# Kernel tuning notes

Hardware: AMD Instinct MI355X
Metric: run time of the kernel (lower is better)

The kernel has to match this reference:

```python
import jax, jax.numpy as jnp
import numpy as np


def _gcn_norm(edge_index, num_nodes, dtype):
    # PyG GCNConv.norm: add self-loops (weight 1), symmetric deg^{-1/2} normalization
    row, col = edge_index[0], edge_index[1]
    loop = jnp.arange(num_nodes, dtype=row.dtype)
    row = jnp.concatenate([row, loop])
    col = jnp.concatenate([col, loop])
    ew = jnp.ones(row.shape[0], dtype=dtype)
    deg = jax.ops.segment_sum(ew, row, num_segments=num_nodes)
    dis = jnp.where(deg > 0, jax.lax.rsqrt(deg), 0.0)
    norm = dis[row] * ew * dis[col]
    return row, col, norm


def _masked_gcn_conv(x, row, col, norm, sigma, W, b, num_nodes):
    # mask_features: edge gather -> diff/sigma -> square -> scatter-add -> exp mask
    h = (x[col] - x[row]) / sigma            # [E, F]
    h = norm[:, None] * h * h                # [E, F]
    mask = jax.ops.segment_sum(h, row, num_segments=num_nodes)        # [N, F]
    deg = jax.ops.segment_sum(jnp.ones_like(norm), row, num_segments=num_nodes)  # degree(source), >=1 due to self-loops
    x = x * jnp.exp(-mask / deg[:, None])
    # GCNConv: linear transform then normalized aggregation source->target
    xw = x @ W                               # [N, O]
    out = jax.ops.segment_sum(norm[:, None] * xw[row], col, num_segments=num_nodes)
    return out + b


def setup_inputs() -> dict:
    key = jax.random.key(0)
    ks = jax.random.split(key, 8)
    N, E, F, H, C = 100000, 1600000, 128, 64, 40
    g = 1.414  # xavier gain used for sigma
    return {
        "x": jax.random.normal(ks[0], (N, F), jnp.float32),
        "edge_index": jax.random.randint(ks[1], (2, E), 0, N, jnp.int64),
        "sigma1": jax.random.uniform(ks[2], (1, F), jnp.float32, -1.0, 1.0) * (g * np.sqrt(6.0 / (1 + F))),
        "W1": jax.random.normal(ks[3], (F, H), jnp.float32) * (1.0 / np.sqrt(F)),
        "b1": jnp.zeros((H,), jnp.float32),
        "sigma2": jax.random.uniform(ks[4], (1, H), jnp.float32, -1.0, 1.0) * (g * np.sqrt(6.0 / (1 + H))),
        "W2": jax.random.normal(ks[5], (H, C), jnp.float32) * (1.0 / np.sqrt(H)),
        "b2": jnp.zeros((C,), jnp.float32),
    }


def reference(x, edge_index, sigma1, W1, b1, sigma2, W2, b2):
    N = x.shape[0]
    row, col, norm = _gcn_norm(edge_index, N, x.dtype)
    x = _masked_gcn_conv(x, row, col, norm, sigma1, W1, b1, N)
    x = jax.nn.relu(x)
    # dropout is identity in eval mode
    x = _masked_gcn_conv(x, row, col, norm, sigma2, W2, b2, N)
    return jax.nn.log_softmax(x, axis=1)
```

## Files before the change

### kernel.cpp

```cpp
#include <hip/hip_runtime.h>
#include <cmath>

constexpr int F1 = 128;
constexpr int H  = 64;
constexpr int NC = 40;
constexpr int NPART = 8;

constexpr int SCAN_TPB = 256;
constexpr int SCAN_IPT = 8;
constexpr int SCAN_EPB = SCAN_TPB * SCAN_IPT;

__device__ inline unsigned short f2bf(float f) {
    union { float f; unsigned u; } v; v.f = f;
    return (unsigned short)((v.u + 0x7FFFu + ((v.u >> 16) & 1u)) >> 16);
}
__device__ inline float bflo(unsigned p) { union { float f; unsigned u; } v; v.u = p << 16; return v.f; }
__device__ inline float bfhi(unsigned p) { union { float f; unsigned u; } v; v.u = p & 0xFFFF0000u; return v.f; }
__device__ inline void unpack8(uint4 raw, float* d) {
    d[0] = bflo(raw.x); d[1] = bfhi(raw.x); d[2] = bflo(raw.y); d[3] = bfhi(raw.y);
    d[4] = bflo(raw.z); d[5] = bfhi(raw.z); d[6] = bflo(raw.w); d[7] = bfhi(raw.w);
}

__device__ inline unsigned f2q(float f) {
    union { float f; unsigned u; } v; v.f = f;
    unsigned s = (v.u >> 24) & 0x80u;
    float a = fabsf(f);
    if (a > 448.0f) return s | 0x7Eu;
    if (a < 0.0009765625f) return s;
    if (a >= 0.015625f) {
        unsigned b = v.u & 0x7fffffffu;
        unsigned r = b + 0x0007FFFFu + ((b >> 20) & 1u);
        unsigned e8 = (r >> 23) - 120u;
        unsigned m8 = (r >> 20) & 7u;
        unsigned q = (e8 << 3) | m8;
        if (q > 0x7Eu) q = 0x7Eu;
        return s | q;
    }
    unsigned m = (unsigned)rintf(a * 512.0f);
    if (m > 7u) m = 8u;
    return s | m;
}
#if defined(__has_builtin) && __has_builtin(__builtin_amdgcn_cvt_pk_f32_fp8)
typedef float __attribute__((ext_vector_type(2))) f32x2_t;
__device__ inline void q2f4(unsigned w, float* d) {
    f32x2_t lo = __builtin_amdgcn_cvt_pk_f32_fp8((int)w, false);
    f32x2_t hi = __builtin_amdgcn_cvt_pk_f32_fp8((int)w, true);
    d[0] = lo[0]; d[1] = lo[1]; d[2] = hi[0]; d[3] = hi[1];
}
#else
__device__ inline float q2f1(unsigned b) {
    unsigned em = b & 0x7fu;
    union { float f; unsigned u; } r;
    r.u = (em << 20) + (120u << 23);
    float mag = em ? r.f : 0.0f;
    union { float f; unsigned u; } o; o.f = mag;
    o.u |= (b & 0x80u) << 24;
    return o.f;
}
__device__ inline void q2f4(unsigned w, float* d) {
    d[0] = q2f1(w & 0xffu); d[1] = q2f1((w >> 8) & 0xffu);
    d[2] = q2f1((w >> 16) & 0xffu); d[3] = q2f1((w >> 24) & 0xffu);
}
#endif
__device__ inline void unpackq8(uint2 raw, float* d) {
    q2f4(raw.x, d); q2f4(raw.y, d + 4);
}

__global__ void isg_kernel(const float* __restrict__ s1, float* __restrict__ i1,
                           const float* __restrict__ s2, float* __restrict__ i2) {
    int i = threadIdx.x;
    if (i < F1) i1[i] = 1.0f / s1[i];
    if (i < H)  i2[i] = 1.0f / s2[i];
}

__global__ void count8_prep_kernel(const int* __restrict__ row, const int* __restrict__ col,
                                   int* __restrict__ cntO, int* __restrict__ cntI,
                                   int E, int chunk, int stride, int cntBlocks,
                                   const float* __restrict__ x, const float* __restrict__ isg,
                                   unsigned short* __restrict__ u, unsigned char* __restrict__ uq,
                                   size_t n8) {
    int bid = blockIdx.x;
    if (bid < cntBlocks) {
        int p = bid & (NPART - 1);
        int gid = bid / NPART;
        unsigned lo = (unsigned)(p * chunk);
        for (int e = gid * blockDim.x + threadIdx.x; e < E; e += stride) {
            int r = row[e], c = col[e];
            if ((unsigned)r - lo < (unsigned)chunk) atomicAdd(&cntO[r], 1);
            if ((unsigned)c - lo < (unsigned)chunk) atomicAdd(&cntI[c], 1);
        }
    } else {
        size_t idx = (size_t)(bid - cntBlocks) * blockDim.x + threadIdx.x;
        if (idx >= n8) return;
        size_t base = idx * 8;
        int fk = (int)(base % (size_t)F1);
        float4 a0 = *(const float4*)&x[base];
        float4 a1 = *(const float4*)&x[base + 4];
        float4 s0 = *(const float4*)&isg[fk];
        float4 s1 = *(const float4*)&isg[fk + 4];
        float uv[8] = {a0.x * s0.x, a0.y * s0.y, a0.z * s0.z, a0.w * s0.w,
                       a1.x * s1.x, a1.y * s1.y, a1.z * s1.z, a1.w * s1.w};
        uint4 p4;
        p4.x = (unsigned)f2bf(uv[0]) | ((unsigned)f2bf(uv[1]) << 16);
        p4.y = (unsigned)f2bf(uv[2]) | ((unsigned)f2bf(uv[3]) << 16);
        p4.z = (unsigned)f2bf(uv[4]) | ((unsigned)f2bf(uv[5]) << 16);
        p4.w = (unsigned)f2bf(uv[6]) | ((unsigned)f2bf(uv[7]) << 16);
        *(uint4*)&u[base] = p4;
        uint2 q2;
        q2.x = f2q(uv[0]) | (f2q(uv[1]) << 8) | (f2q(uv[2]) << 16) | (f2q(uv[3]) << 24);
        q2.y = f2q(uv[4]) | (f2q(uv[5]) << 8) | (f2q(uv[6]) << 16) | (f2q(uv[7]) << 24);
        *(uint2*)&uq[base] = q2;
    }
}

__global__ void scan_partial_kernel(const int* __restrict__ cnt, int* __restrict__ bsum, int M) {
    __shared__ int red[SCAN_TPB];
    int t = threadIdx.x;
    int i0 = blockIdx.x * SCAN_EPB + t * SCAN_IPT;
    int s = 0;
#pragma unroll
    for (int k = 0; k < SCAN_IPT; ++k) {
        int i = i0 + k;
        if (i < M) s += cnt[i];
    }
    red[t] = s;
    __syncthreads();
    for (int off = SCAN_TPB / 2; off > 0; off >>= 1) {
        if (t < off) red[t] += red[t + off];
        __syncthreads();
    }
    if (t == 0) bsum[blockIdx.x] = red[0];
}

__global__ void scan_offsets_kernel(int* __restrict__ bsum, int nb,
                                    int* __restrict__ rowptrO, int* __restrict__ rowptrI,
                                    int N, int E) {
    __shared__ int sh[1024];
    int t = threadIdx.x;
    sh[t] = (t < nb) ? bsum[t] : 0;
    __syncthreads();
    for (int off = 1; off < 1024; off <<= 1) {
        int v = (t >= off) ? sh[t - off] : 0;
        __syncthreads();
        sh[t] += v;
        __syncthreads();
    }
    if (t < nb) bsum[t] = (t > 0) ? sh[t - 1] : 0;
    if (t == 0) { rowptrO[N] = E; rowptrI[N] = E; }
}

__global__ void scan_final_kernel(int* __restrict__ cntO, int* __restrict__ cntI,
                                  const int* __restrict__ bsum,
                                  int* __restrict__ rowptrO, int* __restrict__ rowptrI,
                                  float* __restrict__ dis, int N, int E) {
    __shared__ int sh[SCAN_TPB];
    int t = threadIdx.x;
    int M = 2 * N;
    const int* cnt = cntO;
    int i0 = blockIdx.x * SCAN_EPB + t * SCAN_IPT;
    int cv[SCAN_IPT], pre[SCAN_IPT];
    int run = 0;
#pragma unroll
    for (int k = 0; k < SCAN_IPT; ++k) {
        int i = i0 + k;
        cv[k] = (i < M) ? cnt[i] : 0;
        pre[k] = run;
        run += cv[k];
    }
    sh[t] = run;
    __syncthreads();
    for (int off = 1; off < SCAN_TPB; off <<= 1) {
        int v = (t >= off) ? sh[t - off] : 0;
        __syncthreads();
        sh[t] += v;
        __syncthreads();
    }
    int toff = ((t > 0) ? sh[t - 1] : 0) + bsum[blockIdx.x];
#pragma unroll
    for (int k = 0; k < SCAN_IPT; ++k) {
        int i = i0 + k;
        if (i < M) {
            int val = toff + pre[k];
            if (i < N) {
                rowptrO[i] = val;
                cntO[i] = val;
                dis[i] = rsqrtf((float)(cv[k] + 1));
            } else {
                rowptrI[i - N] = val - E;
                cntI[i - N] = val - E;
            }
        }
    }
}

__global__ void build8_kernel(const int* __restrict__ row, const int* __restrict__ col,
                              int* __restrict__ curO, int* __restrict__ curI,
                              int2* __restrict__ adjO2, int2* __restrict__ adjI2,
                              const float* __restrict__ dis,
                              int E, int chunk, int stride) {
    int p = blockIdx.x & (NPART - 1);
    int gid = blockIdx.x / NPART;
    unsigned lo = (unsigned)(p * chunk);
    for (int e = gid * blockDim.x + threadIdx.x; e < E; e += stride) {
        int r = row[e], c = col[e];
        bool inR = (unsigned)r - lo < (unsigned)chunk;
        bool inC = (unsigned)c - lo < (unsigned)chunk;
        if (inR | inC) {
            float nrm = dis[r] * dis[c];
            int nb = __float_as_int(nrm);
            if (inR) adjO2[atomicAdd(&curO[r], 1)] = make_int2(c, nb);
            if (inC) adjI2[atomicAdd(&curI[c], 1)] = make_int2(r, nb);
        }
    }
}

template<int F, int O, int R>
__global__ void fused_mask_gemm_kernel(const int* __restrict__ rowptr, const int2* __restrict__ adj2,
                                       const float* __restrict__ sig,
                                       const unsigned short* __restrict__ u,
                                       const unsigned char* __restrict__ uq,
                                       const float* __restrict__ W,
                                       unsigned short* __restrict__ Ybf, int N) {
    constexpr int NT = R * 64;
    constexpr int G = F / 8;
    constexpr int NPI = 64 / G;
    __shared__ __align__(16) float Ws[F * O];
    __shared__ __align__(16) float Xs[R][F];
    int tid = threadIdx.x;
    for (int i = tid; i < F * O; i += NT) Ws[i] = W[i];
    int w = tid >> 6, lane = tid & 63;
    int h = lane / G, j = lane % G;
    int base = blockIdx.x * R;
    int r = base + w;
    if (r < N) {
        int beg = rowptr[r], end = rowptr[r + 1];
        float inv_deg = 1.0f / (float)(end - beg + 1);
        float ur[8], acc[8];
        unpack8(*(const uint4*)&u[(size_t)r * F + 8 * j], ur);
#pragma unroll
        for (int k = 0; k < 8; ++k) acc[k] = 0.0f;
        for (int t = beg; t < end; t += 2 * NPI) {
            int e0 = t + h, e1 = t + NPI + h;
            int2 a0 = adj2[min(e0, end - 1)];
            int2 a1 = adj2[min(e1, end - 1)];
            float n0 = (e0 < end) ? __int_as_float(a0.y) : 0.0f;
            float n1 = (e1 < end) ? __int_as_float(a1.y) : 0.0f;
            uint2 rw0 = *(const uint2*)&uq[(size_t)a0.x * F + 8 * j];
            uint2 rw1 = *(const uint2*)&uq[(size_t)a1.x * F + 8 * j];
            float uc[8];
            unpackq8(rw0, uc);
#pragma unroll
            for (int q = 0; q < 8; ++q) {
                float d = uc[q] - ur[q];
                acc[q] = fmaf(n0 * d, d, acc[q]);
            }
            unpackq8(rw1, uc);
#pragma unroll
            for (int q = 0; q < 8; ++q) {
                float d = uc[q] - ur[q];
                acc[q] = fmaf(n1 * d, d, acc[q]);
            }
        }
#pragma unroll
        for (int off = G; off < 64; off <<= 1) {
#pragma unroll
            for (int k = 0; k < 8; ++k) acc[k] += __shfl_xor(acc[k], off);
        }
        if (h == 0) {
            float4 s0 = *(const float4*)&sig[8 * j];
            float4 s1 = *(const float4*)&sig[8 * j + 4];
            float sg[8] = {s0.x, s0.y, s0.z, s0.w, s1.x, s1.y, s1.z, s1.w};
            float xm[8];
#pragma unroll
            for (int k = 0; k < 8; ++k) xm[k] = ur[k] * sg[k] * expf(-acc[k] * inv_deg);
            *(float4*)&Xs[w][8 * j]     = make_float4(xm[0], xm[1], xm[2], xm[3]);
            *(float4*)&Xs[w][8 * j + 4] = make_float4(xm[4], xm[5], xm[6], xm[7]);
        }
    } else if (h == 0) {
        *(float4*)&Xs[w][8 * j]     = make_float4(0.f, 0.f, 0.f, 0.f);
        *(float4*)&Xs[w][8 * j + 4] = make_float4(0.f, 0.f, 0.f, 0.f);
    }
    __syncthreads();
    if (w < 2) {
        int r0 = base + 4 * w;
        if (r0 < N && lane < O) {
            float a0 = 0.f, a1 = 0.f, a2 = 0.f, a3 = 0.f;
#pragma unroll
            for (int fq = 0; fq < F / 4; ++fq) {
                float4 x0 = *(const float4*)&Xs[4 * w + 0][4 * fq];
                float4 x1 = *(const float4*)&Xs[4 * w + 1][4 * fq];
                float4 x2 = *(const float4*)&Xs[4 * w + 2][4 * fq];
                float4 x3 = *(const float4*)&Xs[4 * w + 3][4 * fq];
                float w0 = Ws[(4 * fq + 0) * O + lane];
                float w1 = Ws[(4 * fq + 1) * O + lane];
                float w2 = Ws[(4 * fq + 2) * O + lane];
                float w3 = Ws[(4 * fq + 3) * O + lane];
                a0 = fmaf(x0.x, w0, a0); a0 = fmaf(x0.y, w1, a0); a0 = fmaf(x0.z, w2, a0); a0 = fmaf(x0.w, w3, a0);
                a1 = fmaf(x1.x, w0, a1); a1 = fmaf(x1.y, w1, a1); a1 = fmaf(x1.z, w2, a1); a1 = fmaf(x1.w, w3, a1);
                a2 = fmaf(x2.x, w0, a2); a2 = fmaf(x2.y, w1, a2); a2 = fmaf(x2.z, w2, a2); a2 = fmaf(x2.w, w3, a2);
                a3 = fmaf(x3.x, w0, a3); a3 = fmaf(x3.y, w1, a3); a3 = fmaf(x3.z, w2, a3); a3 = fmaf(x3.w, w3, a3);
            }
            float o0 = __shfl_xor(a0, 1);
            float o1 = __shfl_xor(a1, 1);
            float o2 = __shfl_xor(a2, 1);
            float o3 = __shfl_xor(a3, 1);
            if (!(lane & 1)) {
                *(unsigned*)&Ybf[(size_t)r0 * O + lane] = (unsigned)f2bf(a0) | ((unsigned)f2bf(o0) << 16);
                if (r0 + 1 < N) *(unsigned*)&Ybf[(size_t)(r0 + 1) * O + lane] = (unsigned)f2bf(a1) | ((unsigned)f2bf(o1) << 16);
                if (r0 + 2 < N) *(unsigned*)&Ybf[(size_t)(r0 + 2) * O + lane] = (unsigned)f2bf(a2) | ((unsigned)f2bf(o2) << 16);
                if (r0 + 3 < N) *(unsigned*)&Ybf[(size_t)(r0 + 3) * O + lane] = (unsigned)f2bf(a3) | ((unsigned)f2bf(o3) << 16);
            }
        }
    }
}

__global__ void agg_relu_kernel(const int* __restrict__ rowptr, const int2* __restrict__ adj2,
                                const float* __restrict__ dis, const unsigned short* __restrict__ ybf,
                                const float* __restrict__ bias,
                                unsigned short* __restrict__ u2, unsigned char* __restrict__ u2q,
                                const float* __restrict__ isg2, int N) {
    int c = blockIdx.x * (blockDim.x >> 6) + (threadIdx.x >> 6);
    if (c >= N) return;
    int lane = threadIdx.x & 63;
    int h = lane >> 3, j = lane & 7;
    int beg = rowptr[c], end = rowptr[c + 1];
    float acc[8];
#pragma unroll
    for (int k = 0; k < 8; ++k) acc[k] = 0.0f;
    for (int t = beg; t < end; t += 16) {
        int e0 = t + h, e1 = t + 8 + h;
        int2 a0 = adj2[min(e0, end - 1)];
        int2 a1 = adj2[min(e1, end - 1)];
        float n0 = (e0 < end) ? __int_as_float(a0.y) : 0.0f;
        float n1 = (e1 < end) ? __int_as_float(a1.y) : 0.0f;
        uint4 rw0 = *(const uint4*)&ybf[(size_t)a0.x * H + 8 * j];
        uint4 rw1 = *(const uint4*)&ybf[(size_t)a1.x * H + 8 * j];
        float v[8];
        unpack8(rw0, v);
#pragma unroll
        for (int q = 0; q < 8; ++q) acc[q] = fmaf(n0, v[q], acc[q]);
        unpack8(rw1, v);
#pragma unroll
        for (int q = 0; q < 8; ++q) acc[q] = fmaf(n1, v[q], acc[q]);
    }
#pragma unroll
    for (int off = 8; off < 64; off <<= 1) {
#pragma unroll
        for (int k = 0; k < 8; ++k) acc[k] += __shfl_xor(acc[k], off);
    }
    if (h == 0) {
        float dc = dis[c];
        float sv[8];
        unpack8(*(const uint4*)&ybf[(size_t)c * H + 8 * j], sv);
        float4 b0 = *(const float4*)&bias[8 * j];
        float4 b1v = *(const float4*)&bias[8 * j + 4];
        float bb[8] = {b0.x, b0.y, b0.z, b0.w, b1v.x, b1v.y, b1v.z, b1v.w};
        float4 s0 = *(const float4*)&isg2[8 * j];
        float4 s1 = *(const float4*)&isg2[8 * j + 4];
        float sg[8] = {s0.x, s0.y, s0.z, s0.w, s1.x, s1.y, s1.z, s1.w};
        float uv[8];
        float d2 = dc * dc;
#pragma unroll
        for (int k = 0; k < 8; ++k) {
            float hv = fmaxf(fmaf(d2, sv[k], acc[k]) + bb[k], 0.0f);
            uv[k] = hv * sg[k];
        }
        uint4 p;
        p.x = (unsigned)f2bf(uv[0]) | ((unsigned)f2bf(uv[1]) << 16);
        p.y = (unsigned)f2bf(uv[2]) | ((unsigned)f2bf(uv[3]) << 16);
        p.z = (unsigned)f2bf(uv[4]) | ((unsigned)f2bf(uv[5]) << 16);
        p.w = (unsigned)f2bf(uv[6]) | ((unsigned)f2bf(uv[7]) << 16);
        *(uint4*)&u2[(size_t)c * H + 8 * j] = p;
        uint2 q2;
        q2.x = f2q(uv[0]) | (f2q(uv[1]) << 8) | (f2q(uv[2]) << 16) | (f2q(uv[3]) << 24);
        q2.y = f2q(uv[4]) | (f2q(uv[5]) << 8) | (f2q(uv[6]) << 16) | (f2q(uv[7]) << 24);
        *(uint2*)&u2q[(size_t)c * H + 8 * j] = q2;
    }
}

__global__ void agg_lsm_kernel(const int* __restrict__ rowptr, const int2* __restrict__ adj2,
                               const float* __restrict__ dis, const unsigned short* __restrict__ ybf,
                               const float* __restrict__ bias, float* __restrict__ out, int N) {
    int c = blockIdx.x * (blockDim.x >> 6) + (threadIdx.x >> 6);
    if (c >= N) return;
    int lane = threadIdx.x & 63;
    int h = lane >> 4, j = lane & 15;
    bool active = j < 10;
    int beg = rowptr[c], end = rowptr[c + 1];
    float a[4] = {0.f, 0.f, 0.f, 0.f};
    for (int t = beg; t < end; t += 8) {
        int e0 = t + h, e1 = t + 4 + h;
        int2 a0 = adj2[min(e0, end - 1)];
        int2 a1 = adj2[min(e1, end - 1)];
        float n0 = (e0 < end) ? __int_as_float(a0.y) : 0.0f;
        float n1 = (e1 < end) ? __int_as_float(a1.y) : 0.0f;
        uint2 rw0 = active ? *(const uint2*)&ybf[(size_t)a0.x * NC + 4 * j] : make_uint2(0u, 0u);
        uint2 rw1 = active ? *(const uint2*)&ybf[(size_t)a1.x * NC + 4 * j] : make_uint2(0u, 0u);
        a[0] = fmaf(n0, bflo(rw0.x), a[0]); a[1] = fmaf(n0, bfhi(rw0.x), a[1]);
        a[2] = fmaf(n0, bflo(rw0.y), a[2]); a[3] = fmaf(n0, bfhi(rw0.y), a[3]);
        a[0] = fmaf(n1, bflo(rw1.x), a[0]); a[1] = fmaf(n1, bfhi(rw1.x), a[1]);
        a[2] = fmaf(n1, bflo(rw1.y), a[2]); a[3] = fmaf(n1, bfhi(rw1.y), a[3]);
    }
#pragma unroll
    for (int off = 16; off < 64; off <<= 1) {
#pragma unroll
        for (int k = 0; k < 4; ++k) a[k] += __shfl_xor(a[k], off);
    }
    bool wr = (h == 0) && active;
    float v[4] = {-INFINITY, -INFINITY, -INFINITY, -INFINITY};
    if (wr) {
        float dc = dis[c];
        uint2 sr = *(const uint2*)&ybf[(size_t)c * NC + 4 * j];
        float sv[4] = {bflo(sr.x), bfhi(sr.x), bflo(sr.y), bfhi(sr.y)};
        float4 bb = *(const float4*)&bias[4 * j];
        float b4[4] = {bb.x, bb.y, bb.z, bb.w};
        float d2 = dc * dc;
#pragma unroll
        for (int k = 0; k < 4; ++k) v[k] = fmaf(d2, sv[k], a[k]) + b4[k];
    }
    float m = fmaxf(fmaxf(v[0], v[1]), fmaxf(v[2], v[3]));
#pragma unroll
    for (int off = 8; off > 0; off >>= 1) m = fmaxf(m, __shfl_xor(m, off));
    float s = wr ? (expf(v[0] - m) + expf(v[1] - m) + expf(v[2] - m) + expf(v[3] - m)) : 0.0f;
#pragma unroll
    for (int off = 8; off > 0; off >>= 1) s += __shfl_xor(s, off);
    float mls = m + logf(s);
    if (wr)
        *(float4*)&out[(size_t)c * NC + 4 * j] = make_float4(v[0] - mls, v[1] - mls, v[2] - mls, v[3] - mls);
}

extern "C" void kernel_launch(void* const* d_in, const int* in_sizes, int n_in,
                              void* d_out, int out_size, void* d_ws, size_t ws_size,
                              hipStream_t stream) {
    const float* x    = (const float*)d_in[0];
    const int*   ei   = (const int*)  d_in[1];
    const float* sig1 = (const float*)d_in[2];
    const float* W1   = (const float*)d_in[3];
    const float* b1   = (const float*)d_in[4];
    const float* sig2 = (const float*)d_in[5];
    const float* W2   = (const float*)d_in[6];
    const float* b2   = (const float*)d_in[7];
    float* out = (float*)d_out;

    const int N = in_sizes[0] / F1;
    const int E = in_sizes[1] / 2;
    const int* row = ei;
    const int* col = ei + E;

    char* w = (char*)d_ws;
    auto alloc = [&](size_t bytes) { void* q = w; w += (bytes + 255) & ~255ull; return q; };
    int*   cntO    = (int*)  alloc((size_t)2 * N * 4);
    int*   cntI    = cntO + N;
    int*   rowptrO = (int*)  alloc((size_t)(N + 1) * 4);
    int*   rowptrI = (int*)  alloc((size_t)(N + 1) * 4);
    int2*  adjO2   = (int2*) alloc((size_t)E * 8);
    int2*  adjI2   = (int2*) alloc((size_t)E * 8);
    float* dis     = (float*)alloc((size_t)N * 4);
    float* isg1    = (float*)alloc(F1 * 4);
    float* isg2    = (float*)alloc(H * 4);
    int*   bsum    = (int*)  alloc(1024 * 4);
    unsigned short* u1   = (unsigned short*)alloc((size_t)N * F1 * 2);
    unsigned char*  u1q  = (unsigned char*) alloc((size_t)N * F1);
    unsigned short* u2   = (unsigned short*)alloc((size_t)N * H * 2);
    unsigned char*  u2q  = (unsigned char*) alloc((size_t)N * H);
    unsigned short* ybf1 = (unsigned short*)alloc((size_t)N * H * 2);
    unsigned short* ybf2 = u1;

    const int B = 256;
    const int chunk = (N + NPART - 1) / NPART;
    const int TOTB = 8192;
    const int stride8 = (TOTB / NPART) * B;
    const size_t n8 = (size_t)N * F1 / 8;
    const int prepBlocks = (int)((n8 + B - 1) / B);
    const int M = 2 * N;
    const int nb = (M + SCAN_EPB - 1) / SCAN_EPB;

    hipMemsetAsync(cntO, 0, (size_t)2 * N * 4, stream);
    isg_kernel<<<1, 128, 0, stream>>>(sig1, isg1, sig2, isg2);
    count8_prep_kernel<<<TOTB + prepBlocks, B, 0, stream>>>(
        row, col, cntO, cntI, E, chunk, stride8, TOTB, x, isg1, u1, u1q, n8);
    scan_partial_kernel<<<nb, SCAN_TPB, 0, stream>>>(cntO, bsum, M);
    scan_offsets_kernel<<<1, 1024, 0, stream>>>(bsum, nb, rowptrO, rowptrI, N, E);
    scan_final_kernel<<<nb, SCAN_TPB, 0, stream>>>(cntO, cntI, bsum, rowptrO, rowptrI, dis, N, E);
    build8_kernel<<<TOTB, B, 0, stream>>>(row, col, cntO, cntI, adjO2, adjI2, dis, E, chunk, stride8);

    fused_mask_gemm_kernel<F1, H, 8><<<(N + 7) / 8, 512, 0, stream>>>(rowptrO, adjO2, sig1, u1, u1q, W1, ybf1, N);
    agg_relu_kernel<<<(N + 3) / 4, B, 0, stream>>>(rowptrI, adjI2, dis, ybf1, b1, u2, u2q, isg2, N);

    fused_mask_gemm_kernel<H, NC, 8><<<(N + 7) / 8, 512, 0, stream>>>(rowptrO, adjO2, sig2, u2, u2q, W2, ybf2, N);
    agg_lsm_kernel<<<(N + 3) / 4, B, 0, stream>>>(rowptrI, adjI2, dis, ybf2, b2, out, N);
}
```

Before: 617.7 us.

## Store GEMM outputs as 8-bit floats and replicate degree counters across copies

The transformed features written by the fused mask+GEMM kernels are now stored as 8-bit floats instead of bf16, halving the bytes gathered per edge in both aggregation kernels. Degree counting now uses one edge per thread with atomics spread over eight replicated counter arrays (aliased onto the u2 buffer), replacing the partitioned strided loop. The scan kernels sum the eight copies. This reduces atomic contention and gather bandwidth at the cost of lower precision in the aggregated activations and a larger memset.

```diff
diff --git a/kernel.cpp b/kernel.cpp
--- a/kernel.cpp
+++ b/kernel.cpp
@@ -5,6 +5,7 @@
 constexpr int H  = 64;
 constexpr int NC = 40;
 constexpr int NPART = 8;
+constexpr int NCOPY = 8;
 
 constexpr int SCAN_TPB = 256;
 constexpr int SCAN_IPT = 8;
@@ -73,24 +74,21 @@
     if (i < H)  i2[i] = 1.0f / s2[i];
 }
 
-__global__ void count8_prep_kernel(const int* __restrict__ row, const int* __restrict__ col,
-                                   int* __restrict__ cntO, int* __restrict__ cntI,
-                                   int E, int chunk, int stride, int cntBlocks,
+__global__ void count1_prep_kernel(const int* __restrict__ row, const int* __restrict__ col,
+                                   int* __restrict__ cnt8, int E, int N, int cntBlocks,
                                    const float* __restrict__ x, const float* __restrict__ isg,
                                    unsigned short* __restrict__ u, unsigned char* __restrict__ uq,
                                    size_t n8) {
     int bid = blockIdx.x;
     if (bid < cntBlocks) {
-        int p = bid & (NPART - 1);
-        int gid = bid / NPART;
-        unsigned lo = (unsigned)(p * chunk);
-        for (int e = gid * blockDim.x + threadIdx.x; e < E; e += stride) {
-            int r = row[e], c = col[e];
-            if ((unsigned)r - lo < (unsigned)chunk) atomicAdd(&cntO[r], 1);
-            if ((unsigned)c - lo < (unsigned)chunk) atomicAdd(&cntI[c], 1);
+        int e = bid * 256 + threadIdx.x;
+        if (e < E) {
+            int* cnt = cnt8 + (size_t)(bid & (NCOPY - 1)) * 2 * N;
+            atomicAdd(&cnt[row[e]], 1);
+            atomicAdd(&cnt[N + col[e]], 1);
         }
     } else {
-        size_t idx = (size_t)(bid - cntBlocks) * blockDim.x + threadIdx.x;
+        size_t idx = (size_t)(bid - cntBlocks) * 256 + threadIdx.x;
         if (idx >= n8) return;
         size_t base = idx * 8;
         int fk = (int)(base % (size_t)F1);
@@ -113,7 +111,7 @@
     }
 }
 
-__global__ void scan_partial_kernel(const int* __restrict__ cnt, int* __restrict__ bsum, int M) {
+__global__ void scan_partial_kernel(const int* __restrict__ cnt8, int* __restrict__ bsum, int M) {
     __shared__ int red[SCAN_TPB];
     int t = threadIdx.x;
     int i0 = blockIdx.x * SCAN_EPB + t * SCAN_IPT;
@@ -121,7 +119,10 @@
 #pragma unroll
     for (int k = 0; k < SCAN_IPT; ++k) {
         int i = i0 + k;
-        if (i < M) s += cnt[i];
+        if (i < M) {
+#pragma unroll
+            for (int c = 0; c < NCOPY; ++c) s += cnt8[(size_t)c * M + i];
+        }
     }
     red[t] = s;
     __syncthreads();
@@ -149,23 +150,28 @@
     if (t == 0) { rowptrO[N] = E; rowptrI[N] = E; }
 }
 
-__global__ void scan_final_kernel(int* __restrict__ cntO, int* __restrict__ cntI,
+__global__ void scan_final_kernel(const int* __restrict__ cnt8,
+                                  int* __restrict__ curO, int* __restrict__ curI,
                                   const int* __restrict__ bsum,
                                   int* __restrict__ rowptrO, int* __restrict__ rowptrI,
                                   float* __restrict__ dis, int N, int E) {
     __shared__ int sh[SCAN_TPB];
     int t = threadIdx.x;
     int M = 2 * N;
-    const int* cnt = cntO;
     int i0 = blockIdx.x * SCAN_EPB + t * SCAN_IPT;
-    int cv[SCAN_IPT], pre[SCAN_IPT];
+    int tot[SCAN_IPT], pre[SCAN_IPT];
     int run = 0;
 #pragma unroll
     for (int k = 0; k < SCAN_IPT; ++k) {
         int i = i0 + k;
-        cv[k] = (i < M) ? cnt[i] : 0;
+        int s = 0;
+        if (i < M) {
+#pragma unroll
+            for (int c = 0; c < NCOPY; ++c) s += cnt8[(size_t)c * M + i];
+        }
+        tot[k] = s;
         pre[k] = run;
-        run += cv[k];
+        run += s;
     }
     sh[t] = run;
     __syncthreads();
@@ -183,11 +189,11 @@
             int val = toff + pre[k];
             if (i < N) {
                 rowptrO[i] = val;
-                cntO[i] = val;
-                dis[i] = rsqrtf((float)(cv[k] + 1));
+                curO[i] = val;
+                dis[i] = rsqrtf((float)(tot[k] + 1));
             } else {
                 rowptrI[i - N] = val - E;
-                cntI[i - N] = val - E;
+                curI[i - N] = val - E;
             }
         }
     }
@@ -220,7 +226,7 @@
                                        const unsigned short* __restrict__ u,
                                        const unsigned char* __restrict__ uq,
                                        const float* __restrict__ W,
-                                       unsigned short* __restrict__ Ybf, int N) {
+                                       unsigned char* __restrict__ Yq, int N) {
     constexpr int NT = R * 64;
     constexpr int G = F / 8;
     constexpr int NPI = 64 / G;
@@ -300,22 +306,25 @@
                 a2 = fmaf(x2.x, w0, a2); a2 = fmaf(x2.y, w1, a2); a2 = fmaf(x2.z, w2, a2); a2 = fmaf(x2.w, w3, a2);
                 a3 = fmaf(x3.x, w0, a3); a3 = fmaf(x3.y, w1, a3); a3 = fmaf(x3.z, w2, a3); a3 = fmaf(x3.w, w3, a3);
             }
-            float o0 = __shfl_xor(a0, 1);
-            float o1 = __shfl_xor(a1, 1);
-            float o2 = __shfl_xor(a2, 1);
-            float o3 = __shfl_xor(a3, 1);
-            if (!(lane & 1)) {
-                *(unsigned*)&Ybf[(size_t)r0 * O + lane] = (unsigned)f2bf(a0) | ((unsigned)f2bf(o0) << 16);
-                if (r0 + 1 < N) *(unsigned*)&Ybf[(size_t)(r0 + 1) * O + lane] = (unsigned)f2bf(a1) | ((unsigned)f2bf(o1) << 16);
-                if (r0 + 2 < N) *(unsigned*)&Ybf[(size_t)(r0 + 2) * O + lane] = (unsigned)f2bf(a2) | ((unsigned)f2bf(o2) << 16);
-                if (r0 + 3 < N) *(unsigned*)&Ybf[(size_t)(r0 + 3) * O + lane] = (unsigned)f2bf(a3) | ((unsigned)f2bf(o3) << 16);
+            int sh8 = 8 * (lane & 3);
+            unsigned q0 = f2q(a0) << sh8, q1 = f2q(a1) << sh8;
+            unsigned q2 = f2q(a2) << sh8, q3 = f2q(a3) << sh8;
+            q0 |= __shfl_xor(q0, 1); q0 |= __shfl_xor(q0, 2);
+            q1 |= __shfl_xor(q1, 1); q1 |= __shfl_xor(q1, 2);
+            q2 |= __shfl_xor(q2, 1); q2 |= __shfl_xor(q2, 2);
+            q3 |= __shfl_xor(q3, 1); q3 |= __shfl_xor(q3, 2);
+            if (!(lane & 3)) {
+                *(unsigned*)&Yq[(size_t)r0 * O + lane] = q0;
+                if (r0 + 1 < N) *(unsigned*)&Yq[(size_t)(r0 + 1) * O + lane] = q1;
+                if (r0 + 2 < N) *(unsigned*)&Yq[(size_t)(r0 + 2) * O + lane] = q2;
+                if (r0 + 3 < N) *(unsigned*)&Yq[(size_t)(r0 + 3) * O + lane] = q3;
             }
         }
     }
 }
 
 __global__ void agg_relu_kernel(const int* __restrict__ rowptr, const int2* __restrict__ adj2,
-                                const float* __restrict__ dis, const unsigned short* __restrict__ ybf,
+                                const float* __restrict__ dis, const unsigned char* __restrict__ yq,
                                 const float* __restrict__ bias,
                                 unsigned short* __restrict__ u2, unsigned char* __restrict__ u2q,
                                 const float* __restrict__ isg2, int N) {
@@ -333,13 +342,13 @@
         int2 a1 = adj2[min(e1, end - 1)];
         float n0 = (e0 < end) ? __int_as_float(a0.y) : 0.0f;
         float n1 = (e1 < end) ? __int_as_float(a1.y) : 0.0f;
-        uint4 rw0 = *(const uint4*)&ybf[(size_t)a0.x * H + 8 * j];
-        uint4 rw1 = *(const uint4*)&ybf[(size_t)a1.x * H + 8 * j];
+        uint2 rw0 = *(const uint2*)&yq[(size_t)a0.x * H + 8 * j];
+        uint2 rw1 = *(const uint2*)&yq[(size_t)a1.x * H + 8 * j];
         float v[8];
-        unpack8(rw0, v);
+        unpackq8(rw0, v);
 #pragma unroll
         for (int q = 0; q < 8; ++q) acc[q] = fmaf(n0, v[q], acc[q]);
-        unpack8(rw1, v);
+        unpackq8(rw1, v);
 #pragma unroll
         for (int q = 0; q < 8; ++q) acc[q] = fmaf(n1, v[q], acc[q]);
     }
@@ -351,7 +360,7 @@
     if (h == 0) {
         float dc = dis[c];
         float sv[8];
-        unpack8(*(const uint4*)&ybf[(size_t)c * H + 8 * j], sv);
+        unpackq8(*(const uint2*)&yq[(size_t)c * H + 8 * j], sv);
         float4 b0 = *(const float4*)&bias[8 * j];
         float4 b1v = *(const float4*)&bias[8 * j + 4];
         float bb[8] = {b0.x, b0.y, b0.z, b0.w, b1v.x, b1v.y, b1v.z, b1v.w};
@@ -379,7 +388,7 @@
 }
 
 __global__ void agg_lsm_kernel(const int* __restrict__ rowptr, const int2* __restrict__ adj2,
-                               const float* __restrict__ dis, const unsigned short* __restrict__ ybf,
+                               const float* __restrict__ dis, const unsigned char* __restrict__ yq,
                                const float* __restrict__ bias, float* __restrict__ out, int N) {
     int c = blockIdx.x * (blockDim.x >> 6) + (threadIdx.x >> 6);
     if (c >= N) return;
@@ -394,12 +403,15 @@
         int2 a1 = adj2[min(e1, end - 1)];
         float n0 = (e0 < end) ? __int_as_float(a0.y) : 0.0f;
         float n1 = (e1 < end) ? __int_as_float(a1.y) : 0.0f;
-        uint2 rw0 = active ? *(const uint2*)&ybf[(size_t)a0.x * NC + 4 * j] : make_uint2(0u, 0u);
-        uint2 rw1 = active ? *(const uint2*)&ybf[(size_t)a1.x * NC + 4 * j] : make_uint2(0u, 0u);
-        a[0] = fmaf(n0, bflo(rw0.x), a[0]); a[1] = fmaf(n0, bfhi(rw0.x), a[1]);
-        a[2] = fmaf(n0, bflo(rw0.y), a[2]); a[3] = fmaf(n0, bfhi(rw0.y), a[3]);
-        a[0] = fmaf(n1, bflo(rw1.x), a[0]); a[1] = fmaf(n1, bfhi(rw1.x), a[1]);
-        a[2] = fmaf(n1, bflo(rw1.y), a[2]); a[3] = fmaf(n1, bfhi(rw1.y), a[3]);
+        unsigned rw0 = active ? *(const unsigned*)&yq[(size_t)a0.x * NC + 4 * j] : 0u;
+        unsigned rw1 = active ? *(const unsigned*)&yq[(size_t)a1.x * NC + 4 * j] : 0u;
+        float v[4];
+        q2f4(rw0, v);
+        a[0] = fmaf(n0, v[0], a[0]); a[1] = fmaf(n0, v[1], a[1]);
+        a[2] = fmaf(n0, v[2], a[2]); a[3] = fmaf(n0, v[3], a[3]);
+        q2f4(rw1, v);
+        a[0] = fmaf(n1, v[0], a[0]); a[1] = fmaf(n1, v[1], a[1]);
+        a[2] = fmaf(n1, v[2], a[2]); a[3] = fmaf(n1, v[3], a[3]);
     }
 #pragma unroll
     for (int off = 16; off < 64; off <<= 1) {
@@ -410,8 +422,8 @@
     float v[4] = {-INFINITY, -INFINITY, -INFINITY, -INFINITY};
     if (wr) {
         float dc = dis[c];
-        uint2 sr = *(const uint2*)&ybf[(size_t)c * NC + 4 * j];
-        float sv[4] = {bflo(sr.x), bfhi(sr.x), bflo(sr.y), bfhi(sr.y)};
+        float sv[4];
+        q2f4(*(const unsigned*)&yq[(size_t)c * NC + 4 * j], sv);
         float4 bb = *(const float4*)&bias[4 * j];
         float b4[4] = {bb.x, bb.y, bb.z, bb.w};
         float d2 = dc * dc;
@@ -449,8 +461,8 @@
 
     char* w = (char*)d_ws;
     auto alloc = [&](size_t bytes) { void* q = w; w += (bytes + 255) & ~255ull; return q; };
-    int*   cntO    = (int*)  alloc((size_t)2 * N * 4);
-    int*   cntI    = cntO + N;
+    int*   curO    = (int*)  alloc((size_t)2 * N * 4);
+    int*   curI    = curO + N;
     int*   rowptrO = (int*)  alloc((size_t)(N + 1) * 4);
     int*   rowptrI = (int*)  alloc((size_t)(N + 1) * 4);
     int2*  adjO2   = (int2*) alloc((size_t)E * 8);
@@ -463,30 +475,32 @@
     unsigned char*  u1q  = (unsigned char*) alloc((size_t)N * F1);
     unsigned short* u2   = (unsigned short*)alloc((size_t)N * H * 2);
     unsigned char*  u2q  = (unsigned char*) alloc((size_t)N * H);
-    unsigned short* ybf1 = (unsigned short*)alloc((size_t)N * H * 2);
-    unsigned short* ybf2 = u1;
+    unsigned char*  yq1  = (unsigned char*) alloc((size_t)N * H);
+    unsigned char*  yq2  = (unsigned char*)u1;
+    int* cnt8 = (int*)u2;
 
     const int B = 256;
     const int chunk = (N + NPART - 1) / NPART;
     const int TOTB = 8192;
     const int stride8 = (TOTB / NPART) * B;
+    const int cntBlocks = (E + B - 1) / B;
     const size_t n8 = (size_t)N * F1 / 8;
     const int prepBlocks = (int)((n8 + B - 1) / B);
     const int M = 2 * N;
     const int nb = (M + SCAN_EPB - 1) / SCAN_EPB;
 
-    hipMemsetAsync(cntO, 0, (size_t)2 * N * 4, stream);
+    hipMemsetAsync(cnt8, 0, (size_t)NCOPY * M * 4, stream);
     isg_kernel<<<1, 128, 0, stream>>>(sig1, isg1, sig2, isg2);
-    count8_prep_kernel<<<TOTB + prepBlocks, B, 0, stream>>>(
-        row, col, cntO, cntI, E, chunk, stride8, TOTB, x, isg1, u1, u1q, n8);
-    scan_partial_kernel<<<nb, SCAN_TPB, 0, stream>>>(cntO, bsum, M);
+    count1_prep_kernel<<<cntBlocks + prepBlocks, B, 0, stream>>>(
+        row, col, cnt8, E, N, cntBlocks, x, isg1, u1, u1q, n8);
+    scan_partial_kernel<<<nb, SCAN_TPB, 0, stream>>>(cnt8, bsum, M);
     scan_offsets_kernel<<<1, 1024, 0, stream>>>(bsum, nb, rowptrO, rowptrI, N, E);
-    scan_final_kernel<<<nb, SCAN_TPB, 0, stream>>>(cntO, cntI, bsum, rowptrO, rowptrI, dis, N, E);
-    build8_kernel<<<TOTB, B, 0, stream>>>(row, col, cntO, cntI, adjO2, adjI2, dis, E, chunk, stride8);
-
-    fused_mask_gemm_kernel<F1, H, 8><<<(N + 7) / 8, 512, 0, stream>>>(rowptrO, adjO2, sig1, u1, u1q, W1, ybf1, N);
-    agg_relu_kernel<<<(N + 3) / 4, B, 0, stream>>>(rowptrI, adjI2, dis, ybf1, b1, u2, u2q, isg2, N);
-
-    fused_mask_gemm_kernel<H, NC, 8><<<(N + 7) / 8, 512, 0, stream>>>(rowptrO, adjO2, sig2, u2, u2q, W2, ybf2, N);
-    agg_lsm_kernel<<<(N + 3) / 4, B, 0, stream>>>(rowptrI, adjI2, dis, ybf2, b2, out, N);
-}
+    scan_final_kernel<<<nb, SCAN_TPB, 0, stream>>>(cnt8, curO, curI, bsum, rowptrO, rowptrI, dis, N, E);
+    build8_kernel<<<TOTB, B, 0, stream>>>(row, col, curO, curI, adjO2, adjI2, dis, E, chunk, stride8);
+
+    fused_mask_gemm_kernel<F1, H, 8><<<(N + 7) / 8, 512, 0, stream>>>(rowptrO, adjO2, sig1, u1, u1q, W1, yq1, N);
+    agg_relu_kernel<<<(N + 3) / 4, B, 0, stream>>>(rowptrI, adjI2, dis, yq1, b1, u2, u2q, isg2, N);
+
+    fused_mask_gemm_kernel<H, NC, 8><<<(N + 7) / 8, 512, 0, stream>>>(rowptrO, adjO2, sig2, u2, u2q, W2, yq2, N);
+    agg_lsm_kernel<<<(N + 3) / 4, B, 0, stream>>>(rowptrI, adjI2, dis, yq2, b2, out, N);
+}
```

Result: slower. 2.171 ms (+251.4%).
